# Performance work log

Hardware: AMD Instinct MI355X
Metric: run time of the kernel (lower is better)

## Reference

```python
import jax, jax.numpy as jnp
import numpy as np

N, E, IN_F, H_F, OUT_F = 50000, 800000, 128, 128, 3
BN_EPS = 1e-5


def setup_inputs() -> dict:
    key = jax.random.key(0)
    ks = jax.random.split(key, 8)
    x = jax.random.normal(ks[0], (N, IN_F), dtype=jnp.float32)
    edge_index = jax.random.randint(ks[1], (2, E), 0, N, dtype=jnp.int64)
    edge_weight = jax.random.uniform(ks[2], (E,), dtype=jnp.float32)
    # GCNConv weight (Glorot-style scale) and bias
    conv_w = jax.random.normal(ks[3], (IN_F, H_F), dtype=jnp.float32) * (1.0 / np.sqrt(IN_F))
    conv_b = jnp.zeros((H_F,), dtype=jnp.float32)
    # BatchNorm affine params
    gamma = jnp.ones((H_F,), dtype=jnp.float32)
    beta = jnp.zeros((H_F,), dtype=jnp.float32)
    # Final linear
    lin_w = jax.random.normal(ks[4], (H_F, OUT_F), dtype=jnp.float32) * (1.0 / np.sqrt(H_F))
    lin_b = jnp.zeros((OUT_F,), dtype=jnp.float32)
    return {"x": x, "edge_index": edge_index, "edge_weight": edge_weight,
            "conv_w": conv_w, "conv_b": conv_b, "gamma": gamma, "beta": beta,
            "lin_w": lin_w, "lin_b": lin_b}


def _gcn_conv(x, edge_index, edge_weight, conv_w, conv_b):
    n = x.shape[0]
    # add self-loops with weight 1 (PyG GCNConv default)
    loops = jnp.arange(n, dtype=edge_index.dtype)
    row = jnp.concatenate([edge_index[0], loops])
    col = jnp.concatenate([edge_index[1], loops])
    ew = jnp.concatenate([edge_weight, jnp.ones((n,), dtype=edge_weight.dtype)])
    # symmetric normalization: deg over destination nodes
    deg = jax.ops.segment_sum(ew, col, num_segments=n)
    dinv = jnp.where(deg > 0, jax.lax.rsqrt(deg), 0.0)
    norm = dinv[row] * ew * dinv[col]            # [E+N]
    h = x @ conv_w                                # [N, h_f]
    msg = h[row] * norm[:, None]                  # gather + scale, [E+N, h_f]
    agg = jax.ops.segment_sum(msg, col, num_segments=n)  # scatter-add
    return agg + conv_b


def reference(x, edge_index, edge_weight, conv_w, conv_b, gamma, beta, lin_w, lin_b):
    h = jax.nn.relu(_gcn_conv(x, edge_index, edge_weight, conv_w, conv_b))
    # BatchNorm1d over the node dimension (training-style batch stats, biased var)
    mean = jnp.mean(h, axis=0)
    var = jnp.mean((h - mean) ** 2, axis=0)
    hn = (h - mean) * jax.lax.rsqrt(var + BN_EPS) * gamma + beta
    # dropout is identity (deterministic eval-style reference)
    return hn @ lin_w + lin_b
```

## Files before the change

### kernel.cpp

```cpp
#include <hip/hip_runtime.h>

#define NN   50000
#define NE   800000
#define FH   128
#define NOUT 3
#define BN_EPS 1e-5f

#define CAP  64
#define EWS  65535.0f
#define IEWS (1.0f / 65535.0f)
#define FXS  8388608.0f

#define GEMM_BLKS   782
#define BUCKET_BLKS 391
#define STAT_BLKS   256

#define WS_H2      0
#define WS_AGG2    3200000
#define WS_BUCKET  6400000
#define WS_PACKED  9600000
#define WS_DINV    9700000
#define WS_PARTIAL 9750000
#define WS_PREP    9815552

typedef __attribute__((ext_vector_type(8))) short  short8;
typedef __attribute__((ext_vector_type(4))) float  f32x4;

__device__ __forceinline__ unsigned int pack_bf16(float a, float b) {
    unsigned int ua = __float_as_uint(a);
    unsigned int ub = __float_as_uint(b);
    ua += 0x7fffu + ((ua >> 16) & 1u);
    ub += 0x7fffu + ((ub >> 16) & 1u);
    return (ua >> 16) | (ub & 0xffff0000u);
}
__device__ __forceinline__ unsigned short bf16_1(float a) {
    unsigned int ua = __float_as_uint(a);
    ua += 0x7fffu + ((ua >> 16) & 1u);
    return (unsigned short)(ua >> 16);
}
__device__ __forceinline__ float bf16_lo(unsigned int u) {
    return __uint_as_float(u << 16);
}
__device__ __forceinline__ float bf16_hi(unsigned int u) {
    return __uint_as_float(u & 0xffff0000u);
}

__global__ __launch_bounds__(256) void k_bucket(const int* __restrict__ ei,
                                                const float* __restrict__ ew,
                                                unsigned long long* __restrict__ packed,
                                                unsigned int* __restrict__ bucket) {
    const int e0 = blockIdx.x * 2048 + threadIdx.x;
    int                col[8];
    unsigned int       ent[8];
    unsigned long long add[8];
    int                ok[8];
#pragma unroll
    for (int k = 0; k < 8; ++k) {
        int e = e0 + k * 256;
        ok[k] = (e < NE);
        int ee = ok[k] ? e : 0;
        int row = ei[ee];
        col[k] = ei[NE + ee];
        float wv = ew[ee];
        ent[k] = ((unsigned int)row << 16) | __float2uint_rn(wv * EWS);
        add[k] = (1ULL << 32) | (unsigned long long)__float2uint_rn(wv * FXS);
    }
    int slot[8];
#pragma unroll
    for (int k = 0; k < 8; ++k)
        slot[k] = ok[k] ? (int)(atomicAdd(&packed[col[k]], add[k]) >> 32) : 0;
#pragma unroll
    for (int k = 0; k < 8; ++k)
        if (ok[k]) bucket[(size_t)col[k] * CAP + slot[k]] = ent[k];
}

__global__ __launch_bounds__(256) void k_gemm(const float* __restrict__ x,
                                              const float* __restrict__ w,
                                              unsigned int* __restrict__ h2,
                                              const unsigned long long* __restrict__ packed,
                                              float* __restrict__ dinv) {
    __shared__ unsigned short swB[32 * 64 * 8];
    const int tid = threadIdx.x;

    {
        int gi = blockIdx.x * 256 + tid;
        if (gi < NN) {
            unsigned int lo = (unsigned int)(packed[gi] & 0xffffffffu);
            dinv[gi] = rsqrtf((float)lo * (1.0f / FXS) + 1.0f);
        }
    }

#pragma unroll
    for (int it = 0; it < 8; ++it) {
        int s  = tid + it * 256;
        int l  = s & 63;
        int fs = s >> 6;
        int kc = fs >> 3, t = fs & 7;
        int n  = (l & 15) + 16 * t;
        int k0 = kc * 32 + (l >> 4) * 8;
        unsigned short* dst = &swB[s * 8];
#pragma unroll
        for (int j = 0; j < 8; ++j)
            dst[j] = bf16_1(w[(size_t)(k0 + j) * FH + n]);
    }
    __syncthreads();

    const int wv = tid >> 6, l = tid & 63;
    const int m = l & 15, q = l >> 4;
    int node = blockIdx.x * 64 + wv * 16 + m;
    if (node >= NN) node = NN - 1;

    f32x4 acc[8];
#pragma unroll
    for (int t = 0; t < 8; ++t) acc[t] = (f32x4){0.f, 0.f, 0.f, 0.f};

#pragma unroll
    for (int kc = 0; kc < 4; ++kc) {
        const float* xr = x + (size_t)node * FH + kc * 32 + q * 8;
        float4 a0 = *(const float4*)xr;
        float4 a1 = *(const float4*)(xr + 4);
        union { short8 s8; uint4 u4; } af;
        af.u4.x = pack_bf16(a0.x, a0.y);  af.u4.y = pack_bf16(a0.z, a0.w);
        af.u4.z = pack_bf16(a1.x, a1.y);  af.u4.w = pack_bf16(a1.z, a1.w);
#pragma unroll
        for (int t = 0; t < 8; ++t) {
            union { short8 s8; uint4 u4; } bf;
            bf.u4 = *(const uint4*)&swB[((kc * 8 + t) * 64 + l) * 8];
            acc[t] = __builtin_amdgcn_mfma_f32_16x16x32_bf16(af.s8, bf.s8, acc[t], 0, 0, 0);
        }
    }

    __syncthreads();
    unsigned short* sc = swB;
#pragma unroll
    for (int t = 0; t < 8; ++t) {
#pragma unroll
        for (int r = 0; r < 4; ++r) {
            int ml = wv * 16 + q * 4 + r;
            int f  = t * 16 + m;
            sc[ml * FH + f] = bf16_1(acc[t][r]);
        }
    }
    __syncthreads();
    const uint4* s4 = (const uint4*)sc;
#pragma unroll
    for (int i = 0; i < 4; ++i) {
        int u  = tid + i * 256;
        int nl = u >> 4;
        int ng = blockIdx.x * 64 + nl;
        if (ng < NN)
            *((uint4*)h2 + (size_t)ng * 16 + (u & 15)) = s4[u];
    }
}

__global__ __launch_bounds__(256) void k_gather(const unsigned int* __restrict__ h2,
                                                const float* __restrict__ dinv,
                                                const unsigned int* __restrict__ bucket,
                                                const unsigned long long* __restrict__ packed,
                                                const float* __restrict__ conv_b,
                                                unsigned int* __restrict__ agg2) {
    int n = blockIdx.x * 4 + (threadIdx.x >> 6);
    int lane = threadIdx.x & 63;

    float dvn = dinv[n];
    unsigned int hself = h2[(size_t)n * 64 + lane];
    float ax = bf16_lo(hself) * dvn;
    float ay = bf16_hi(hself) * dvn;

    const unsigned int* bkt = bucket + (size_t)n * CAP;
    int c = (int)(packed[n] >> 32);
    int j = 0;
    for (; j + 8 <= c; j += 8) {
        uint4 b0 = *(const uint4*)(bkt + j);
        uint4 b1 = *(const uint4*)(bkt + j + 4);
        unsigned int u[8] = {b0.x, b0.y, b0.z, b0.w, b1.x, b1.y, b1.z, b1.w};
        float t[8];
        unsigned int q[8];
#pragma unroll
        for (int r = 0; r < 8; ++r) {
            int s = u[r] >> 16;
            t[r] = dinv[s] * (float)(u[r] & 0xffffu) * IEWS;
            q[r] = h2[(size_t)s * 64 + lane];
        }
#pragma unroll
        for (int r = 0; r < 8; ++r) {
            ax = fmaf(bf16_lo(q[r]), t[r], ax);
            ay = fmaf(bf16_hi(q[r]), t[r], ay);
        }
    }
    if (j + 4 <= c) {
        uint4 b0 = *(const uint4*)(bkt + j);
        unsigned int u[4] = {b0.x, b0.y, b0.z, b0.w};
#pragma unroll
        for (int r = 0; r < 4; ++r) {
            int s = u[r] >> 16;
            float t = dinv[s] * (float)(u[r] & 0xffffu) * IEWS;
            unsigned int q = h2[(size_t)s * 64 + lane];
            ax = fmaf(bf16_lo(q), t, ax);
            ay = fmaf(bf16_hi(q), t, ay);
        }
        j += 4;
    }
    for (; j < c; ++j) {
        unsigned int u0 = bkt[j];
        int s0 = u0 >> 16;
        float t0 = dinv[s0] * (float)(u0 & 0xffffu) * IEWS;
        unsigned int q0 = h2[(size_t)s0 * 64 + lane];
        ax = fmaf(bf16_lo(q0), t0, ax);  ay = fmaf(bf16_hi(q0), t0, ay);
    }

    float2 bv = *(const float2*)(conv_b + lane * 2);
    float ox = fmaxf(fmaf(dvn, ax, bv.x), 0.f);
    float oy = fmaxf(fmaf(dvn, ay, bv.y), 0.f);
    agg2[(size_t)n * 64 + lane] = pack_bf16(ox, oy);
}

__global__ __launch_bounds__(256) void k_stats(const unsigned int* __restrict__ agg2,
                                               float* __restrict__ partial) {
    int c2 = threadIdx.x & 31;
    int g  = threadIdx.x >> 5;
    float s[4]  = {0.f, 0.f, 0.f, 0.f};
    float s2[4] = {0.f, 0.f, 0.f, 0.f};
    for (int n = blockIdx.x * 8 + g; n < NN; n += STAT_BLKS * 8) {
        uint2 v = *(const uint2*)(agg2 + (size_t)n * 64 + c2 * 2);
        float a0 = bf16_lo(v.x), a1 = bf16_hi(v.x);
        float a2 = bf16_lo(v.y), a3 = bf16_hi(v.y);
        s[0] += a0;  s2[0] = fmaf(a0, a0, s2[0]);
        s[1] += a1;  s2[1] = fmaf(a1, a1, s2[1]);
        s[2] += a2;  s2[2] = fmaf(a2, a2, s2[2]);
        s[3] += a3;  s2[3] = fmaf(a3, a3, s2[3]);
    }
    __shared__ float red[256];
    float* pb = partial + (size_t)blockIdx.x * 256;
#pragma unroll
    for (int r = 0; r < 8; ++r) {
        red[threadIdx.x] = (r < 4) ? s[r] : s2[r - 4];
        __syncthreads();
        if (g == 0) {
            float t = 0.f;
#pragma unroll
            for (int gg = 0; gg < 8; ++gg) t += red[c2 + 32 * gg];
            pb[((r < 4) ? 0 : FH) + 4 * c2 + (r & 3)] = t;
        }
        __syncthreads();
    }
}

__global__ void k_prep(const float* __restrict__ partial,
                       const float* __restrict__ gamma,
                       const float* __restrict__ beta,
                       const float* __restrict__ lin_w,
                       const float* __restrict__ lin_b,
                       float* __restrict__ prep) {
    __shared__ float ssum[256];
    __shared__ float red[3 * FH];
    int i = threadIdx.x;
    float acc = 0.f;
    for (int b = 0; b < STAT_BLKS; ++b) acc += partial[(size_t)b * 256 + i];
    ssum[i] = acc;
    __syncthreads();
    if (i < FH) {
        float mean = ssum[i] * (1.0f / NN);
        float var  = ssum[FH + i] * (1.0f / NN) - mean * mean;
        float inv  = rsqrtf(var + BN_EPS);
        float sc   = inv * gamma[i];
        float sh   = fmaf(-mean, sc, beta[i]);
#pragma unroll
        for (int o = 0; o < NOUT; ++o) {
            float lw = lin_w[i * NOUT + o];
            prep[i * NOUT + o] = sc * lw;
            red[o * FH + i]    = sh * lw;
        }
    }
    __syncthreads();
    if (i < NOUT) {
        float s = lin_b[i];
        for (int f = 0; f < FH; ++f) s += red[i * FH + f];
        prep[3 * FH + i] = s;
    }
}

__global__ __launch_bounds__(256) void k_final(const unsigned int* __restrict__ agg2,
                                               const float* __restrict__ prep,
                                               float* __restrict__ out) {
    int n = blockIdx.x * 4 + (threadIdx.x >> 6);
    int lane = threadIdx.x & 63;
    int f0 = lane * 2, f1 = lane * 2 + 1;

    unsigned int v = agg2[(size_t)n * 64 + lane];
    float vx = bf16_lo(v), vy = bf16_hi(v);

    float o0 = vx * prep[f0 * NOUT + 0] + vy * prep[f1 * NOUT + 0];
    float o1 = vx * prep[f0 * NOUT + 1] + vy * prep[f1 * NOUT + 1];
    float o2 = vx * prep[f0 * NOUT + 2] + vy * prep[f1 * NOUT + 2];

#pragma unroll
    for (int off = 32; off > 0; off >>= 1) {
        o0 += __shfl_down(o0, off, 64);
        o1 += __shfl_down(o1, off, 64);
        o2 += __shfl_down(o2, off, 64);
    }
    if (lane == 0) {
        out[n * NOUT + 0] = o0 + prep[3 * FH + 0];
        out[n * NOUT + 1] = o1 + prep[3 * FH + 1];
        out[n * NOUT + 2] = o2 + prep[3 * FH + 2];
    }
}

extern "C" void kernel_launch(void* const* d_in, const int* in_sizes, int n_in,
                              void* d_out, int out_size, void* d_ws, size_t ws_size,
                              hipStream_t stream) {
    const float* x      = (const float*)d_in[0];
    const int*   ei     = (const int*)d_in[1];
    const float* ew     = (const float*)d_in[2];
    const float* conv_w = (const float*)d_in[3];
    const float* conv_b = (const float*)d_in[4];
    const float* gamma  = (const float*)d_in[5];
    const float* beta   = (const float*)d_in[6];
    const float* lin_w  = (const float*)d_in[7];
    const float* lin_b  = (const float*)d_in[8];
    float* out = (float*)d_out;
    float* ws  = (float*)d_ws;

    unsigned int*       h2      = (unsigned int*)(ws + WS_H2);
    unsigned int*       agg2    = (unsigned int*)(ws + WS_AGG2);
    unsigned int*       bucket  = (unsigned int*)(ws + WS_BUCKET);
    unsigned long long* packed  = (unsigned long long*)(ws + WS_PACKED);
    float*              dinv    = ws + WS_DINV;
    float*              partial = ws + WS_PARTIAL;
    float*              prep    = ws + WS_PREP;

    hipMemsetAsync(packed, 0, (size_t)NN * sizeof(unsigned long long), stream);

    k_bucket<<<BUCKET_BLKS, 256, 0, stream>>>(ei, ew, packed, bucket);
    k_gemm  <<<GEMM_BLKS,   256, 0, stream>>>(x, conv_w, h2, packed, dinv);
    k_gather<<<NN / 4,      256, 0, stream>>>(h2, dinv, bucket, packed, conv_b, agg2);
    k_stats <<<STAT_BLKS,   256, 0, stream>>>(agg2, partial);
    k_prep  <<<1,           256, 0, stream>>>(partial, gamma, beta, lin_w, lin_b, prep);
    k_final <<<NN / 4,      256, 0, stream>>>(agg2, prep, out);
}
```

Measured before the change: 199.7 us.

## Fuse BatchNorm statistics into gather kernel with grid-stride loop and two-stage reduction

The gather kernel now runs a grid-stride loop over nodes and accumulates per-feature sums and sums of squares in registers. This removes the separate stats kernel and its re-read of agg2. A new k_red kernel reduces the 2048 per-block partials into 8 rows, which k_prep then sums. Bucket capacity drops from 64 to 48 and the bucket kernel uses more blocks with fewer edges per thread. The lower capacity risks overflow for high in-degree nodes, and the fixed gather grid may cut the parallelism available for hiding latency.

```diff
diff --git a/kernel.cpp b/kernel.cpp
--- a/kernel.cpp
+++ b/kernel.cpp
@@ -6,22 +6,24 @@
 #define NOUT 3
 #define BN_EPS 1e-5f
 
-#define CAP  64
+#define CAP  48
 #define EWS  65535.0f
 #define IEWS (1.0f / 65535.0f)
 #define FXS  8388608.0f
 
 #define GEMM_BLKS   782
-#define BUCKET_BLKS 391
-#define STAT_BLKS   256
+#define BUCKET_BLKS 782
+#define GATHER_BLKS 2048
+#define RED_BLKS    (GATHER_BLKS / 256)
 
 #define WS_H2      0
 #define WS_AGG2    3200000
 #define WS_BUCKET  6400000
-#define WS_PACKED  9600000
-#define WS_DINV    9700000
-#define WS_PARTIAL 9750000
-#define WS_PREP    9815552
+#define WS_PACKED  8800000
+#define WS_DINV    8900000
+#define WS_PARTIAL 8950000
+#define WS_STAGE2  9474288
+#define WS_PREP    9476336
 
 typedef __attribute__((ext_vector_type(8))) short  short8;
 typedef __attribute__((ext_vector_type(4))) float  f32x4;
@@ -49,13 +51,13 @@
                                                 const float* __restrict__ ew,
                                                 unsigned long long* __restrict__ packed,
                                                 unsigned int* __restrict__ bucket) {
-    const int e0 = blockIdx.x * 2048 + threadIdx.x;
-    int                col[8];
-    unsigned int       ent[8];
-    unsigned long long add[8];
-    int                ok[8];
-#pragma unroll
-    for (int k = 0; k < 8; ++k) {
+    const int e0 = blockIdx.x * 1024 + threadIdx.x;
+    int                col[4];
+    unsigned int       ent[4];
+    unsigned long long add[4];
+    int                ok[4];
+#pragma unroll
+    for (int k = 0; k < 4; ++k) {
         int e = e0 + k * 256;
         ok[k] = (e < NE);
         int ee = ok[k] ? e : 0;
@@ -65,12 +67,12 @@
         ent[k] = ((unsigned int)row << 16) | __float2uint_rn(wv * EWS);
         add[k] = (1ULL << 32) | (unsigned long long)__float2uint_rn(wv * FXS);
     }
-    int slot[8];
-#pragma unroll
-    for (int k = 0; k < 8; ++k)
+    int slot[4];
+#pragma unroll
+    for (int k = 0; k < 4; ++k)
         slot[k] = ok[k] ? (int)(atomicAdd(&packed[col[k]], add[k]) >> 32) : 0;
 #pragma unroll
-    for (int k = 0; k < 8; ++k)
+    for (int k = 0; k < 4; ++k)
         if (ok[k]) bucket[(size_t)col[k] * CAP + slot[k]] = ent[k];
 }
 
@@ -158,95 +160,95 @@
                                                 const unsigned int* __restrict__ bucket,
                                                 const unsigned long long* __restrict__ packed,
                                                 const float* __restrict__ conv_b,
-                                                unsigned int* __restrict__ agg2) {
-    int n = blockIdx.x * 4 + (threadIdx.x >> 6);
-    int lane = threadIdx.x & 63;
-
-    float dvn = dinv[n];
-    unsigned int hself = h2[(size_t)n * 64 + lane];
-    float ax = bf16_lo(hself) * dvn;
-    float ay = bf16_hi(hself) * dvn;
-
-    const unsigned int* bkt = bucket + (size_t)n * CAP;
-    int c = (int)(packed[n] >> 32);
-    int j = 0;
-    for (; j + 8 <= c; j += 8) {
-        uint4 b0 = *(const uint4*)(bkt + j);
-        uint4 b1 = *(const uint4*)(bkt + j + 4);
-        unsigned int u[8] = {b0.x, b0.y, b0.z, b0.w, b1.x, b1.y, b1.z, b1.w};
-        float t[8];
-        unsigned int q[8];
-#pragma unroll
-        for (int r = 0; r < 8; ++r) {
-            int s = u[r] >> 16;
-            t[r] = dinv[s] * (float)(u[r] & 0xffffu) * IEWS;
-            q[r] = h2[(size_t)s * 64 + lane];
-        }
-#pragma unroll
-        for (int r = 0; r < 8; ++r) {
-            ax = fmaf(bf16_lo(q[r]), t[r], ax);
-            ay = fmaf(bf16_hi(q[r]), t[r], ay);
-        }
-    }
-    if (j + 4 <= c) {
-        uint4 b0 = *(const uint4*)(bkt + j);
-        unsigned int u[4] = {b0.x, b0.y, b0.z, b0.w};
-#pragma unroll
-        for (int r = 0; r < 4; ++r) {
-            int s = u[r] >> 16;
-            float t = dinv[s] * (float)(u[r] & 0xffffu) * IEWS;
-            unsigned int q = h2[(size_t)s * 64 + lane];
-            ax = fmaf(bf16_lo(q), t, ax);
-            ay = fmaf(bf16_hi(q), t, ay);
-        }
-        j += 4;
-    }
-    for (; j < c; ++j) {
-        unsigned int u0 = bkt[j];
-        int s0 = u0 >> 16;
-        float t0 = dinv[s0] * (float)(u0 & 0xffffu) * IEWS;
-        unsigned int q0 = h2[(size_t)s0 * 64 + lane];
-        ax = fmaf(bf16_lo(q0), t0, ax);  ay = fmaf(bf16_hi(q0), t0, ay);
-    }
-
+                                                unsigned int* __restrict__ agg2,
+                                                float* __restrict__ partial) {
+    const int lane = threadIdx.x & 63;
+    const int wv   = threadIdx.x >> 6;
     float2 bv = *(const float2*)(conv_b + lane * 2);
-    float ox = fmaxf(fmaf(dvn, ax, bv.x), 0.f);
-    float oy = fmaxf(fmaf(dvn, ay, bv.y), 0.f);
-    agg2[(size_t)n * 64 + lane] = pack_bf16(ox, oy);
-}
-
-__global__ __launch_bounds__(256) void k_stats(const unsigned int* __restrict__ agg2,
-                                               float* __restrict__ partial) {
-    int c2 = threadIdx.x & 31;
-    int g  = threadIdx.x >> 5;
-    float s[4]  = {0.f, 0.f, 0.f, 0.f};
-    float s2[4] = {0.f, 0.f, 0.f, 0.f};
-    for (int n = blockIdx.x * 8 + g; n < NN; n += STAT_BLKS * 8) {
-        uint2 v = *(const uint2*)(agg2 + (size_t)n * 64 + c2 * 2);
-        float a0 = bf16_lo(v.x), a1 = bf16_hi(v.x);
-        float a2 = bf16_lo(v.y), a3 = bf16_hi(v.y);
-        s[0] += a0;  s2[0] = fmaf(a0, a0, s2[0]);
-        s[1] += a1;  s2[1] = fmaf(a1, a1, s2[1]);
-        s[2] += a2;  s2[2] = fmaf(a2, a2, s2[2]);
-        s[3] += a3;  s2[3] = fmaf(a3, a3, s2[3]);
-    }
+
+    float sa = 0.f, sb = 0.f, sa2 = 0.f, sb2 = 0.f;
+
+    for (int n = blockIdx.x * 4 + wv; n < NN; n += GATHER_BLKS * 4) {
+        float dvn = dinv[n];
+        unsigned int hself = h2[(size_t)n * 64 + lane];
+        float ax = bf16_lo(hself) * dvn;
+        float ay = bf16_hi(hself) * dvn;
+
+        const unsigned int* bkt = bucket + (size_t)n * CAP;
+        int c = (int)(packed[n] >> 32);
+        int j = 0;
+        for (; j + 8 <= c; j += 8) {
+            uint4 b0 = *(const uint4*)(bkt + j);
+            uint4 b1 = *(const uint4*)(bkt + j + 4);
+            unsigned int u[8] = {b0.x, b0.y, b0.z, b0.w, b1.x, b1.y, b1.z, b1.w};
+            float t[8];
+            unsigned int q[8];
+#pragma unroll
+            for (int r = 0; r < 8; ++r) {
+                int s = u[r] >> 16;
+                t[r] = dinv[s] * (float)(u[r] & 0xffffu) * IEWS;
+                q[r] = h2[(size_t)s * 64 + lane];
+            }
+#pragma unroll
+            for (int r = 0; r < 8; ++r) {
+                ax = fmaf(bf16_lo(q[r]), t[r], ax);
+                ay = fmaf(bf16_hi(q[r]), t[r], ay);
+            }
+        }
+        if (j + 4 <= c) {
+            uint4 b0 = *(const uint4*)(bkt + j);
+            unsigned int u[4] = {b0.x, b0.y, b0.z, b0.w};
+#pragma unroll
+            for (int r = 0; r < 4; ++r) {
+                int s = u[r] >> 16;
+                float t = dinv[s] * (float)(u[r] & 0xffffu) * IEWS;
+                unsigned int q = h2[(size_t)s * 64 + lane];
+                ax = fmaf(bf16_lo(q), t, ax);
+                ay = fmaf(bf16_hi(q), t, ay);
+            }
+            j += 4;
+        }
+        for (; j < c; ++j) {
+            unsigned int u0 = bkt[j];
+            int s0 = u0 >> 16;
+            float t0 = dinv[s0] * (float)(u0 & 0xffffu) * IEWS;
+            unsigned int q0 = h2[(size_t)s0 * 64 + lane];
+            ax = fmaf(bf16_lo(q0), t0, ax);  ay = fmaf(bf16_hi(q0), t0, ay);
+        }
+
+        float ox = fmaxf(fmaf(dvn, ax, bv.x), 0.f);
+        float oy = fmaxf(fmaf(dvn, ay, bv.y), 0.f);
+        agg2[(size_t)n * 64 + lane] = pack_bf16(ox, oy);
+
+        sa += ox;  sa2 = fmaf(ox, ox, sa2);
+        sb += oy;  sb2 = fmaf(oy, oy, sb2);
+    }
+
     __shared__ float red[256];
+    float vals[4] = {sa, sb, sa2, sb2};
     float* pb = partial + (size_t)blockIdx.x * 256;
 #pragma unroll
-    for (int r = 0; r < 8; ++r) {
-        red[threadIdx.x] = (r < 4) ? s[r] : s2[r - 4];
+    for (int r = 0; r < 4; ++r) {
+        red[threadIdx.x] = vals[r];
         __syncthreads();
-        if (g == 0) {
-            float t = 0.f;
-#pragma unroll
-            for (int gg = 0; gg < 8; ++gg) t += red[c2 + 32 * gg];
-            pb[((r < 4) ? 0 : FH) + 4 * c2 + (r & 3)] = t;
+        if (wv == 0) {
+            float t = red[lane] + red[lane + 64] + red[lane + 128] + red[lane + 192];
+            pb[((r < 2) ? 0 : FH) + 2 * lane + (r & 1)] = t;
         }
         __syncthreads();
     }
 }
 
-__global__ void k_prep(const float* __restrict__ partial,
+__global__ __launch_bounds__(256) void k_red(const float* __restrict__ partial,
+                                             float* __restrict__ stage2) {
+    int i = threadIdx.x;
+    const float* base = partial + (size_t)blockIdx.x * 256 * 256;
+    float acc = 0.f;
+    for (int j = 0; j < 256; ++j) acc += base[j * 256 + i];
+    stage2[blockIdx.x * 256 + i] = acc;
+}
+
+__global__ void k_prep(const float* __restrict__ stage2,
                        const float* __restrict__ gamma,
                        const float* __restrict__ beta,
                        const float* __restrict__ lin_w,
@@ -256,7 +258,8 @@
     __shared__ float red[3 * FH];
     int i = threadIdx.x;
     float acc = 0.f;
-    for (int b = 0; b < STAT_BLKS; ++b) acc += partial[(size_t)b * 256 + i];
+#pragma unroll
+    for (int r = 0; r < RED_BLKS; ++r) acc += stage2[r * 256 + i];
     ssum[i] = acc;
     __syncthreads();
     if (i < FH) {
@@ -328,14 +331,15 @@
     unsigned long long* packed  = (unsigned long long*)(ws + WS_PACKED);
     float*              dinv    = ws + WS_DINV;
     float*              partial = ws + WS_PARTIAL;
+    float*              stage2  = ws + WS_STAGE2;
     float*              prep    = ws + WS_PREP;
 
     hipMemsetAsync(packed, 0, (size_t)NN * sizeof(unsigned long long), stream);
 
     k_bucket<<<BUCKET_BLKS, 256, 0, stream>>>(ei, ew, packed, bucket);
     k_gemm  <<<GEMM_BLKS,   256, 0, stream>>>(x, conv_w, h2, packed, dinv);
-    k_gather<<<NN / 4,      256, 0, stream>>>(h2, dinv, bucket, packed, conv_b, agg2);
-    k_stats <<<STAT_BLKS,   256, 0, stream>>>(agg2, partial);
-    k_prep  <<<1,           256, 0, stream>>>(partial, gamma, beta, lin_w, lin_b, prep);
+    k_gather<<<GATHER_BLKS, 256, 0, stream>>>(h2, dinv, bucket, packed, conv_b, agg2, partial);
+    k_red   <<<RED_BLKS,    256, 0, stream>>>(partial, stage2);
+    k_prep  <<<1,           256, 0, stream>>>(stage2, gamma, beta, lin_w, lin_b, prep);
     k_final <<<NN / 4,      256, 0, stream>>>(agg2, prep, out);
 }
```

Result: faster. 194.6 us (-2.5%).
